# Kernel optimization log

Measured on AMD Instinct MI355X. Metric: run time of the kernel, lower is better.

Reference implementation:

```python
import jax, jax.numpy as jnp
import numpy as np

EPS = 1e-8  # torch.nn.CosineSimilarity eps


def setup_inputs() -> dict:
    key = jax.random.key(0)
    k1, k2, k3 = jax.random.split(key, 3)
    C, S, D = 1024, 16, 512
    x = jax.random.normal(k1, (C, S, D), dtype=jnp.float32)
    w = jax.random.normal(k2, (1,), dtype=jnp.float32)
    b = jax.random.normal(k3, (1,), dtype=jnp.float32)
    return {"x": x, "w": w, "b": b}


def reference(x, w, b):
    # stable_ge2e: leave-one-out positive centroids, full negative centroids.
    C, S, D = x.shape
    wp = jax.nn.softplus(w)  # (1,)

    sum_c = x.sum(axis=1)                      # (C, D)
    mean_c = sum_c / S                         # negative centroids (C, D)
    loo = (sum_c[:, None, :] - x) / (S - 1.0)  # leave-one-out centroids (C, S, D)

    nx = jnp.linalg.norm(x, axis=-1)           # (C, S)
    nmean = jnp.linalg.norm(mean_c, axis=-1)   # (C,)
    nloo = jnp.linalg.norm(loo, axis=-1)       # (C, S)

    # cosine similarities (clamped denominator, as in torch CosineSimilarity)
    sim_neg = jnp.einsum('jid,kd->jik', x, mean_c) / jnp.maximum(
        nx[:, :, None] * nmean[None, None, :], EPS)          # (C, S, C)
    sim_pos = jnp.einsum('jid,jid->ji', x, loo) / jnp.maximum(nx * nloo, EPS)  # (C, S)

    # on the diagonal k == j use the leave-one-out positive centroid
    eye = jnp.eye(C, dtype=bool)
    sim = jnp.where(eye[:, None, :], sim_pos[:, :, None], sim_neg)  # (C, S, C)

    logits = wp * sim + b
    logS = jax.nn.log_softmax(logits, axis=-1)
    Sji_j = jnp.einsum('jij->ji', logS)                        # (C, S) diagonal
    Sji_k = jax.scipy.special.logsumexp(logS, axis=-1)         # (C, S) (== 0 post-softmax)
    loss = -(Sji_j - Sji_k).reshape(-1)
    return loss.mean()
```

## Files before the change

kernel.cpp:

```cpp
#include <hip/hip_runtime.h>
#include <math.h>

#define CC 1024
#define SS 16
#define DD 512
#define RR (CC*SS)
#define EPSV 1e-8f
#define LDB 520
#define CHUNK 32
#define NCHUNK 16

typedef __attribute__((ext_vector_type(8))) short short8;
typedef __attribute__((ext_vector_type(4))) float f32x4;
typedef unsigned short ushort_t;

__device__ __forceinline__ unsigned short f2bf(float f) {
  unsigned u = __float_as_uint(f);
  u += 0x7fffu + ((u >> 16) & 1u);
  return (unsigned short)(u >> 16);
}

__device__ __forceinline__ void async16(void* l, const void* g) {
  __builtin_amdgcn_global_load_lds(
      (const __attribute__((address_space(1))) void*)g,
      (__attribute__((address_space(3))) void*)l, 16, 0, 0);
}

__device__ __forceinline__ float softplusf(float v) {
  return (v > 20.f) ? v : log1pf(expf(v));
}

#define SBAR()   __builtin_amdgcn_s_barrier()
#define SCHED0() __builtin_amdgcn_sched_barrier(0)

__global__ __launch_bounds__(256) void k_pre(
    const float* __restrict__ x, ushort_t* __restrict__ mn,
    float* __restrict__ nx, float* __restrict__ simpos,
    ushort_t* __restrict__ xn) {
  __shared__ float xs[SS * DD];
  __shared__ float sums[DD];
  __shared__ float red[4];
  __shared__ float snm;
  __shared__ float rinv[SS];
  const int j = blockIdx.x, tid = threadIdx.x;
  const int wid = tid >> 6, lane = tid & 63;
  const float4* xj = (const float4*)(x + (size_t)j * SS * DD);
  float4* xs4 = (float4*)xs;
#pragma unroll
  for (int t = 0; t < 8; ++t) xs4[tid + t * 256] = xj[tid + t * 256];
  __syncthreads();

  float sx = 0.f, sy = 0.f;
  const float2* xs2 = (const float2*)xs;
#pragma unroll
  for (int i = 0; i < SS; ++i) {
    float2 v = xs2[i * (DD / 2) + tid];
    sx += v.x; sy += v.y;
  }
  ((float2*)sums)[tid] = make_float2(sx, sy);
  const float mxs = sx * (1.0f / SS), mys = sy * (1.0f / SS);
  float m2 = mxs * mxs + mys * mys;
#pragma unroll
  for (int off = 32; off > 0; off >>= 1) m2 += __shfl_xor(m2, off, 64);
  if (lane == 0) red[wid] = m2;
  __syncthreads();
  if (tid == 0) snm = sqrtf(red[0] + red[1] + red[2] + red[3]);
  __syncthreads();
  const float inm = (1.0f / SS) / snm;
  {
    unsigned lo = f2bf(sx * inm), hi = f2bf(sy * inm);
    ((unsigned*)(mn + (size_t)j * DD))[tid] = lo | (hi << 16);
  }

  {
    const int g = tid >> 4, l16 = tid & 15;
    float nx2 = 0.f, dxs = 0.f, t2 = 0.f;
    const float2* xr2 = (const float2*)(xs + g * DD);
    const float2* sm2 = (const float2*)sums;
#pragma unroll
    for (int t = 0; t < 16; ++t) {
      float2 xv = xr2[l16 + t * 16];
      float2 sc = sm2[l16 + t * 16];
      nx2 = fmaf(xv.x, xv.x, fmaf(xv.y, xv.y, nx2));
      dxs = fmaf(xv.x, sc.x, fmaf(xv.y, sc.y, dxs));
      float tx = sc.x - xv.x, ty = sc.y - xv.y;
      t2 = fmaf(tx, tx, fmaf(ty, ty, t2));
    }
#pragma unroll
    for (int off = 1; off < 16; off <<= 1) {
      nx2 += __shfl_xor(nx2, off, 64);
      dxs += __shfl_xor(dxs, off, 64);
      t2  += __shfl_xor(t2,  off, 64);
    }
    if (l16 == 0) {
      float nxv = sqrtf(nx2);
      float tn  = sqrtf(t2);
      float num = (dxs - nx2) * (1.0f / (SS - 1));
      float den = fmaxf(nxv * tn * (1.0f / (SS - 1)), EPSV);
      nx[j * SS + g] = nxv;
      rinv[g] = 1.0f / nxv;
      simpos[j * SS + g] = num / den;
    }
  }
  __syncthreads();
  if (xn) {
    uint2* dst = (uint2*)(xn + (size_t)j * SS * DD);
    const float4* src4 = (const float4*)xs;
#pragma unroll
    for (int t = 0; t < 8; ++t) {
      const int idx = tid + t * 256;
      const float ri = rinv[idx >> 7];
      float4 v = src4[idx];
      uint2 o;
      o.x = (unsigned)f2bf(v.x * ri) | ((unsigned)f2bf(v.y * ri) << 16);
      o.y = (unsigned)f2bf(v.z * ri) | ((unsigned)f2bf(v.w * ri) << 16);
      dst[idx] = o;
    }
  }
}

template <bool USE_XN>
__global__ __launch_bounds__(128, 2) void k_gemm(
    const float* __restrict__ x, const ushort_t* __restrict__ xn,
    const ushort_t* __restrict__ mn, const float* __restrict__ nx,
    const float* __restrict__ simpos, const float* __restrict__ wptr,
    const float* __restrict__ bptr, float* __restrict__ ps) {
  __shared__ ushort_t bs[2][CHUNK * LDB];
  const int tid = threadIdx.x;
  const int wid = tid >> 6, lane = tid & 63;
  const int cL = lane & 15, quad = lane >> 4;
  const int bid = (int)blockIdx.x;
  const int rb = bid & 255, cb = bid >> 8;
  const int r0 = rb * 64, cbase = cb * 512;
  const float wp = softplusf(wptr[0]), bv = bptr[0];
  const int row0w = r0 + wid * 32;

  short8 af[2][16];
  int jw[2];
  float sp[2][4], sacc[2][4];
#pragma unroll
  for (int rt = 0; rt < 2; ++rt) {
    const int row = row0w + rt * 16 + cL;
    if (USE_XN) {
      const short8* src = (const short8*)(xn + (size_t)row * DD);
#pragma unroll
      for (int kc = 0; kc < 16; ++kc) af[rt][kc] = src[kc * 4 + quad];
    } else {
      const float* xr = x + (size_t)row * DD;
      const float invn = 1.0f / nx[row];
#pragma unroll
      for (int kc = 0; kc < 16; ++kc) {
        const int k0 = kc * 32 + quad * 8;
        float4 p = *(const float4*)(xr + k0);
        float4 q = *(const float4*)(xr + k0 + 4);
        short8 v;
        v[0] = f2bf(p.x * invn); v[1] = f2bf(p.y * invn);
        v[2] = f2bf(p.z * invn); v[3] = f2bf(p.w * invn);
        v[4] = f2bf(q.x * invn); v[5] = f2bf(q.y * invn);
        v[6] = f2bf(q.z * invn); v[7] = f2bf(q.w * invn);
        af[rt][kc] = v;
      }
    }
    jw[rt] = (row0w + rt * 16) >> 4;
#pragma unroll
    for (int r = 0; r < 4; ++r) {
      sp[rt][r] = simpos[row0w + rt * 16 + quad * 4 + r];
      sacc[rt][r] = 0.f;
    }
  }

  {
    const ushort_t* gsrc = mn + (size_t)cbase * DD;
#pragma unroll
    for (int t = 0; t < 16; ++t) {
      const int rr = wid + t * 2;
      async16(&bs[0][rr * LDB + lane * 8], gsrc + (size_t)rr * DD + lane * 8);
    }
  }

#pragma unroll
  for (int cc = 0; cc < NCHUNK; ++cc) {
    if (cc < NCHUNK - 1) {
      const ushort_t* gsrc = mn + (size_t)(cbase + (cc + 1) * CHUNK) * DD;
      ushort_t* dst = bs[(cc + 1) & 1];
#pragma unroll
      for (int t = 0; t < 16; ++t) {
        const int rr = wid + t * 2;
        async16(&dst[rr * LDB + lane * 8], gsrc + (size_t)rr * DD + lane * 8);
      }
      SCHED0();
      asm volatile("s_waitcnt vmcnt(16)" ::: "memory");
    } else {
      asm volatile("s_waitcnt vmcnt(0)" ::: "memory");
    }
    SCHED0();
    SBAR();
    SCHED0();

    const ushort_t* B = bs[cc & 1];
    f32x4 acc[2][2];
#pragma unroll
    for (int rt = 0; rt < 2; ++rt)
#pragma unroll
      for (int f = 0; f < 2; ++f) acc[rt][f] = (f32x4){0.f, 0.f, 0.f, 0.f};
#pragma unroll
    for (int kc = 0; kc < 16; ++kc) {
      short8 bfr[2];
#pragma unroll
      for (int f = 0; f < 2; ++f)
        bfr[f] = *(const short8*)&B[(f * 16 + cL) * LDB + kc * 32 + quad * 8];
#pragma unroll
      for (int rt = 0; rt < 2; ++rt)
#pragma unroll
        for (int f = 0; f < 2; ++f)
          acc[rt][f] = __builtin_amdgcn_mfma_f32_16x16x32_bf16(
              af[rt][kc], bfr[f], acc[rt][f], 0, 0, 0);
    }
    const int c0 = cbase + cc * CHUNK;
#pragma unroll
    for (int rt = 0; rt < 2; ++rt)
#pragma unroll
      for (int f = 0; f < 2; ++f) {
        const int cg = c0 + f * 16 + cL;
        const bool diag = (cg == jw[rt]);
#pragma unroll
        for (int r = 0; r < 4; ++r) {
          const float sim = diag ? sp[rt][r] : acc[rt][f][r];
          sacc[rt][r] += __expf(fmaf(wp, sim, bv));
        }
      }
    if (cc < NCHUNK - 1) {
      SCHED0();
      SBAR();
      SCHED0();
    }
  }

#pragma unroll
  for (int rt = 0; rt < 2; ++rt)
#pragma unroll
    for (int r = 0; r < 4; ++r) {
      float v = sacc[rt][r];
#pragma unroll
      for (int off = 1; off < 16; off <<= 1) v += __shfl_xor(v, off, 64);
      if (cL == 0)
        ps[(size_t)(row0w + rt * 16 + quad * 4 + r) * 2 + cb] = v;
    }
}

__global__ __launch_bounds__(1024) void k_loss(
    const float* __restrict__ ps, const float* __restrict__ simpos,
    const float* __restrict__ wptr, const float* __restrict__ bptr,
    float* __restrict__ out) {
  __shared__ float red[16];
  const int tid = threadIdx.x;
  const float wp = softplusf(wptr[0]), bv = bptr[0];
  float acc = 0.f;
#pragma unroll
  for (int i = 0; i < RR / 1024; ++i) {
    const int row = i * 1024 + tid;
    const float2 v = ((const float2*)ps)[row];
    acc += logf(v.x + v.y) - fmaf(wp, simpos[row], bv);
  }
#pragma unroll
  for (int off = 32; off > 0; off >>= 1) acc += __shfl_xor(acc, off, 64);
  if ((tid & 63) == 0) red[tid >> 6] = acc;
  __syncthreads();
  if (tid < 64) {
    float v = (tid < 16) ? red[tid] : 0.f;
#pragma unroll
    for (int off = 8; off > 0; off >>= 1) v += __shfl_xor(v, off, 64);
    if (tid == 0) out[0] = v * (1.0f / RR);
  }
}

extern "C" void kernel_launch(void* const* d_in, const int* in_sizes, int n_in,
                              void* d_out, int out_size, void* d_ws, size_t ws_size,
                              hipStream_t stream) {
  const float* x = (const float*)d_in[0];
  const float* w = (const float*)d_in[1];
  const float* b = (const float*)d_in[2];
  float* out = (float*)d_out;

  const size_t xn_bytes = (size_t)RR * DD * 2;
  const size_t rest = (size_t)CC * DD * 2 + (size_t)RR * 4 * 2 +
                      (size_t)RR * 2 * 4;
  const bool use_xn = ws_size >= xn_bytes + rest + 256;

  char* base = (char*)d_ws;
  ushort_t* xn = use_xn ? (ushort_t*)base : nullptr;
  char* p = base + (use_xn ? xn_bytes : 0);
  ushort_t* mn = (ushort_t*)p;  p += (size_t)CC * DD * 2;
  float* nx     = (float*)p;    p += (size_t)RR * 4;
  float* simpos = (float*)p;    p += (size_t)RR * 4;
  float* ps     = (float*)p;

  k_pre<<<CC, 256, 0, stream>>>(x, mn, nx, simpos, xn);
  if (use_xn)
    k_gemm<true><<<512, 128, 0, stream>>>(x, xn, mn, nx, simpos, w, b, ps);
  else
    k_gemm<false><<<512, 128, 0, stream>>>(x, xn, mn, nx, simpos, w, b, ps);
  k_loss<<<1, 1024, 0, stream>>>(ps, simpos, w, b, out);
}
```

Before: 113.2 us.

## Store normalized x in MFMA fragment order and prefetch centroids earlier

The pre-kernel now writes the bf16 normalized rows in the exact per-lane fragment order the GEMM consumes, so each wave's A-fragment loads become contiguous 16-byte loads per lane instead of strided row loads. The shared staging tile is padded (row stride 516 floats) to reduce LDS bank conflicts when gathering columns across rows during that reordering. The first async centroid chunk load is moved ahead of the A-fragment loads to overlap it with them. This adds coupling between the two kernels' layouts; the non-XN path keeps the old row layout.

```diff
diff --git a/kernel.cpp b/kernel.cpp
--- a/kernel.cpp
+++ b/kernel.cpp
@@ -7,6 +7,7 @@
 #define RR (CC*SS)
 #define EPSV 1e-8f
 #define LDB 520
+#define LDX 516
 #define CHUNK 32
 #define NCHUNK 16
 
@@ -37,7 +38,7 @@
     const float* __restrict__ x, ushort_t* __restrict__ mn,
     float* __restrict__ nx, float* __restrict__ simpos,
     ushort_t* __restrict__ xn) {
-  __shared__ float xs[SS * DD];
+  __shared__ float xs[SS * LDX];
   __shared__ float sums[DD];
   __shared__ float red[4];
   __shared__ float snm;
@@ -45,16 +46,18 @@
   const int j = blockIdx.x, tid = threadIdx.x;
   const int wid = tid >> 6, lane = tid & 63;
   const float4* xj = (const float4*)(x + (size_t)j * SS * DD);
-  float4* xs4 = (float4*)xs;
-#pragma unroll
-  for (int t = 0; t < 8; ++t) xs4[tid + t * 256] = xj[tid + t * 256];
+#pragma unroll
+  for (int t = 0; t < 8; ++t) {
+    const int idx = tid + t * 256;
+    const int row = idx >> 7, d4 = idx & 127;
+    *(float4*)(xs + row * LDX + d4 * 4) = xj[idx];
+  }
   __syncthreads();
 
   float sx = 0.f, sy = 0.f;
-  const float2* xs2 = (const float2*)xs;
 #pragma unroll
   for (int i = 0; i < SS; ++i) {
-    float2 v = xs2[i * (DD / 2) + tid];
+    float2 v = *(const float2*)(xs + i * LDX + tid * 2);
     sx += v.x; sy += v.y;
   }
   ((float2*)sums)[tid] = make_float2(sx, sy);
@@ -75,7 +78,7 @@
   {
     const int g = tid >> 4, l16 = tid & 15;
     float nx2 = 0.f, dxs = 0.f, t2 = 0.f;
-    const float2* xr2 = (const float2*)(xs + g * DD);
+    const float2* xr2 = (const float2*)(xs + g * LDX);
     const float2* sm2 = (const float2*)sums;
 #pragma unroll
     for (int t = 0; t < 16; ++t) {
@@ -104,17 +107,21 @@
   }
   __syncthreads();
   if (xn) {
-    uint2* dst = (uint2*)(xn + (size_t)j * SS * DD);
-    const float4* src4 = (const float4*)xs;
-#pragma unroll
-    for (int t = 0; t < 8; ++t) {
-      const int idx = tid + t * 256;
-      const float ri = rinv[idx >> 7];
-      float4 v = src4[idx];
-      uint2 o;
-      o.x = (unsigned)f2bf(v.x * ri) | ((unsigned)f2bf(v.y * ri) << 16);
-      o.y = (unsigned)f2bf(v.z * ri) | ((unsigned)f2bf(v.w * ri) << 16);
-      dst[idx] = o;
+    uint4* dst = (uint4*)xn + (size_t)j * 1024;
+#pragma unroll
+    for (int t = 0; t < 4; ++t) {
+      const int idxu = tid + t * 256;
+      const int kc = idxu >> 6, quad = (idxu >> 4) & 3, cL = idxu & 15;
+      const float* s = xs + cL * LDX + kc * 32 + quad * 8;
+      const float4 a = *(const float4*)s;
+      const float4 b2 = *(const float4*)(s + 4);
+      const float ri = rinv[cL];
+      uint4 o;
+      o.x = (unsigned)f2bf(a.x * ri) | ((unsigned)f2bf(a.y * ri) << 16);
+      o.y = (unsigned)f2bf(a.z * ri) | ((unsigned)f2bf(a.w * ri) << 16);
+      o.z = (unsigned)f2bf(b2.x * ri) | ((unsigned)f2bf(b2.y * ri) << 16);
+      o.w = (unsigned)f2bf(b2.z * ri) | ((unsigned)f2bf(b2.w * ri) << 16);
+      dst[idxu] = o;
     }
   }
 }
@@ -135,17 +142,27 @@
   const float wp = softplusf(wptr[0]), bv = bptr[0];
   const int row0w = r0 + wid * 32;
 
+  {
+    const ushort_t* gsrc = mn + (size_t)cbase * DD;
+#pragma unroll
+    for (int t = 0; t < 16; ++t) {
+      const int rr = wid + t * 2;
+      async16(&bs[0][rr * LDB + lane * 8], gsrc + (size_t)rr * DD + lane * 8);
+    }
+  }
+
   short8 af[2][16];
   int jw[2];
   float sp[2][4], sacc[2][4];
 #pragma unroll
   for (int rt = 0; rt < 2; ++rt) {
-    const int row = row0w + rt * 16 + cL;
+    jw[rt] = (row0w + rt * 16) >> 4;
     if (USE_XN) {
-      const short8* src = (const short8*)(xn + (size_t)row * DD);
-#pragma unroll
-      for (int kc = 0; kc < 16; ++kc) af[rt][kc] = src[kc * 4 + quad];
+      const short8* xw = (const short8*)xn + (size_t)jw[rt] * 1024;
+#pragma unroll
+      for (int kc = 0; kc < 16; ++kc) af[rt][kc] = xw[kc * 64 + lane];
     } else {
+      const int row = row0w + rt * 16 + cL;
       const float* xr = x + (size_t)row * DD;
       const float invn = 1.0f / nx[row];
 #pragma unroll
@@ -161,20 +178,10 @@
         af[rt][kc] = v;
       }
     }
-    jw[rt] = (row0w + rt * 16) >> 4;
 #pragma unroll
     for (int r = 0; r < 4; ++r) {
       sp[rt][r] = simpos[row0w + rt * 16 + quad * 4 + r];
       sacc[rt][r] = 0.f;
-    }
-  }
-
-  {
-    const ushort_t* gsrc = mn + (size_t)cbase * DD;
-#pragma unroll
-    for (int t = 0; t < 16; ++t) {
-      const int rr = wid + t * 2;
-      async16(&bs[0][rr * LDB + lane * 8], gsrc + (size_t)rr * DD + lane * 8);
     }
   }
 
```

New measurement: 111.0 us. 2.0% less time.
